# Performance work log

Hardware: AMD Instinct MI355X
Metric: run time of the kernel (lower is better)

## Reference

```python
import jax, jax.numpy as jnp
import numpy as np

TROPICAL_ZERO = jnp.float32(-1e38)  # tropical additive identity (acts as -inf)


def setup_inputs() -> dict:
    key = jax.random.key(0)
    k_x, k_w = jax.random.split(key)
    B, IN, OUT = 4096, 256, 256
    x = jax.random.normal(k_x, (B, IN), dtype=jnp.float32)
    # weight = log(rand + 1e-6), matching nn.Parameter init in the torch module
    weight = jnp.log(jax.random.uniform(k_w, (OUT, IN), dtype=jnp.float32) + 1e-6)
    bias = jnp.zeros((OUT,), dtype=jnp.float32)
    return {"x": x, "weight": weight, "bias": bias}


def reference(x, weight, bias):
    # Tropical (max-plus) matmul: out[b, j] = max_k (x[b, k] + w[j, k]) + bias[j]
    # restricted to 'non-tropical-zero' products; if all products are tropical
    # zero, the output stays TROPICAL_ZERO (no bias added), as in the torch loop.
    products = x[:, None, :] + weight[None, :, :]          # [B, out, in]
    mask = products > TROPICAL_ZERO                        # [B, out, in]
    masked = jnp.where(mask, products, -jnp.inf)
    max_val = jnp.max(masked, axis=-1)                     # [B, out]
    any_valid = jnp.any(mask, axis=-1)                     # [B, out]
    out = jnp.where(any_valid, max_val + bias[None, :], TROPICAL_ZERO)
    return out
```

## Files before the change

kernel.cpp:

```cpp
#include <hip/hip_runtime.h>


#define TZERO -1e38f

constexpr int K    = 256;
constexpr int N    = 256;
constexpr int Bdim = 4096;
constexpr int BN   = 32;
constexpr int SKW  = 8;
constexpr int KQ   = K / SKW;
constexpr int NT   = 64 * SKW;
constexpr int RPB  = 64;

__global__ __launch_bounds__(NT, 4)
void tropical_kernel(const float* __restrict__ x, const float* __restrict__ w,
                     const float* __restrict__ bias, float* __restrict__ out)
{
    __shared__ float red[SKW][BN][65];

    const int t    = threadIdx.x;
    const int lane = t & 63;
    const int wave = __builtin_amdgcn_readfirstlane(t >> 6);
    const int row0 = blockIdx.x * RPB;
    const int col0 = blockIdx.y * BN;

    float xr[KQ];
    {
        const float* xp = x + (size_t)(row0 + lane) * K + wave * KQ;
#pragma unroll
        for (int i4 = 0; i4 < KQ / 4; ++i4) {
            const float4 v = *reinterpret_cast<const float4*>(xp + i4 * 4);
            xr[i4 * 4 + 0] = v.x;
            xr[i4 * 4 + 1] = v.y;
            xr[i4 * 4 + 2] = v.z;
            xr[i4 * 4 + 3] = v.w;
        }
    }

    const float* wp0 = w + (size_t)col0 * K + wave * KQ;

#pragma unroll 2
    for (int j = 0; j < BN; ++j) {
        const float* wp = wp0 + (size_t)j * K;
        float m = -__builtin_inff();
#pragma unroll
        for (int i4 = 0; i4 < KQ / 4; ++i4) {
            const float4 wv = *reinterpret_cast<const float4*>(wp + i4 * 4);
            const float t0 = xr[i4 * 4 + 0] + wv.x;
            const float t1 = xr[i4 * 4 + 1] + wv.y;
            const float t2 = xr[i4 * 4 + 2] + wv.z;
            const float t3 = xr[i4 * 4 + 3] + wv.w;
            m = fmaxf(fmaxf(m, t0), t1);
            m = fmaxf(fmaxf(m, t2), t3);
        }
        red[wave][j][lane] = m;
    }
    __syncthreads();

    const int jj = t & 31;
    const int r0 = t >> 5;
    const float bj = bias[col0 + jj];
#pragma unroll
    for (int i = 0; i < 4; ++i) {
        const int r = r0 + 16 * i;
        float m = red[0][jj][r];
#pragma unroll
        for (int q = 1; q < SKW; ++q) m = fmaxf(m, red[q][jj][r]);
        out[(size_t)(row0 + r) * N + col0 + jj] = (m > TZERO) ? m + bj : TZERO;
    }
}

extern "C" void kernel_launch(void* const* d_in, const int* in_sizes, int n_in,
                              void* d_out, int out_size, void* d_ws, size_t ws_size,
                              hipStream_t stream) {
    const float* x  = (const float*)d_in[0];
    const float* w  = (const float*)d_in[1];
    const float* b  = (const float*)d_in[2];
    float* out      = (float*)d_out;

    dim3 grid(Bdim / RPB, N / BN);
    tropical_kernel<<<grid, NT, 0, stream>>>(x, w, b, out);
}
```

Baseline: 74.67 us.

## Shrink column tile to eight and fully unroll per-block column loop

```diff
diff --git a/kernel.cpp b/kernel.cpp
--- a/kernel.cpp
+++ b/kernel.cpp
@@ -6,68 +6,73 @@
 constexpr int K    = 256;
 constexpr int N    = 256;
 constexpr int Bdim = 4096;
-constexpr int BN   = 32;
-constexpr int SKW  = 8;
-constexpr int KQ   = K / SKW;
-constexpr int NT   = 64 * SKW;
-constexpr int RPB  = 64;
+constexpr int ROWS = 64;
+constexpr int J    = 8;
+constexpr int SK   = 8;
+constexpr int KC   = K / SK;
+constexpr int NT   = 64 * SK;
 
-__global__ __launch_bounds__(NT, 4)
+__global__ __launch_bounds__(NT, 8)
 void tropical_kernel(const float* __restrict__ x, const float* __restrict__ w,
                      const float* __restrict__ bias, float* __restrict__ out)
 {
-    __shared__ float red[SKW][BN][65];
+    __shared__ float red[SK][ROWS][J + 1];
 
     const int t    = threadIdx.x;
     const int lane = t & 63;
-    const int wave = __builtin_amdgcn_readfirstlane(t >> 6);
-    const int row0 = blockIdx.x * RPB;
-    const int col0 = blockIdx.y * BN;
+    const int kc   = __builtin_amdgcn_readfirstlane(t >> 6);
+    const int row0 = blockIdx.x * ROWS;
+    const int col0 = blockIdx.y * J;
 
-    float xr[KQ];
+    float xv[KC];
     {
-        const float* xp = x + (size_t)(row0 + lane) * K + wave * KQ;
+        const float* xp = x + (size_t)(row0 + lane) * K + kc * KC;
 #pragma unroll
-        for (int i4 = 0; i4 < KQ / 4; ++i4) {
+        for (int i4 = 0; i4 < KC / 4; ++i4) {
             const float4 v = *reinterpret_cast<const float4*>(xp + i4 * 4);
-            xr[i4 * 4 + 0] = v.x;
-            xr[i4 * 4 + 1] = v.y;
-            xr[i4 * 4 + 2] = v.z;
-            xr[i4 * 4 + 3] = v.w;
+            xv[i4 * 4 + 0] = v.x;
+            xv[i4 * 4 + 1] = v.y;
+            xv[i4 * 4 + 2] = v.z;
+            xv[i4 * 4 + 3] = v.w;
         }
     }
 
-    const float* wp0 = w + (size_t)col0 * K + wave * KQ;
+    float acc[J];
+#pragma unroll
+    for (int j = 0; j < J; ++j) acc[j] = -__builtin_inff();
 
-#pragma unroll 2
-    for (int j = 0; j < BN; ++j) {
-        const float* wp = wp0 + (size_t)j * K;
-        float m = -__builtin_inff();
+    const float* wbase = w + (size_t)col0 * K + kc * KC;
 #pragma unroll
-        for (int i4 = 0; i4 < KQ / 4; ++i4) {
-            const float4 wv = *reinterpret_cast<const float4*>(wp + i4 * 4);
-            const float t0 = xr[i4 * 4 + 0] + wv.x;
-            const float t1 = xr[i4 * 4 + 1] + wv.y;
-            const float t2 = xr[i4 * 4 + 2] + wv.z;
-            const float t3 = xr[i4 * 4 + 3] + wv.w;
+    for (int j = 0; j < J; ++j) {
+        const float* wp = wbase + (size_t)j * K;
+        float m = acc[j];
+#pragma unroll
+        for (int i4 = 0; i4 < KC / 4; ++i4) {
+            const float w0 = wp[i4 * 4 + 0];
+            const float w1 = wp[i4 * 4 + 1];
+            const float w2 = wp[i4 * 4 + 2];
+            const float w3 = wp[i4 * 4 + 3];
+            const float t0 = xv[i4 * 4 + 0] + w0;
+            const float t1 = xv[i4 * 4 + 1] + w1;
+            const float t2 = xv[i4 * 4 + 2] + w2;
+            const float t3 = xv[i4 * 4 + 3] + w3;
             m = fmaxf(fmaxf(m, t0), t1);
             m = fmaxf(fmaxf(m, t2), t3);
         }
-        red[wave][j][lane] = m;
+        acc[j] = m;
     }
+
+#pragma unroll
+    for (int j = 0; j < J; ++j) red[kc][lane][j] = acc[j];
     __syncthreads();
 
-    const int jj = t & 31;
-    const int r0 = t >> 5;
+    const int jj = t & (J - 1);
+    const int r  = t >> 3;
+    float m = red[0][r][jj];
+#pragma unroll
+    for (int q = 1; q < SK; ++q) m = fmaxf(m, red[q][r][jj]);
     const float bj = bias[col0 + jj];
-#pragma unroll
-    for (int i = 0; i < 4; ++i) {
-        const int r = r0 + 16 * i;
-        float m = red[0][jj][r];
-#pragma unroll
-        for (int q = 1; q < SKW; ++q) m = fmaxf(m, red[q][jj][r]);
-        out[(size_t)(row0 + r) * N + col0 + jj] = (m > TZERO) ? m + bj : TZERO;
-    }
+    out[(size_t)(row0 + r) * N + col0 + jj] = (m > TZERO) ? m + bj : TZERO;
 }
 
 extern "C" void kernel_launch(void* const* d_in, const int* in_sizes, int n_in,
@@ -78,6 +83,6 @@
     const float* b  = (const float*)d_in[2];
     float* out      = (float*)d_out;
 
-    dim3 grid(Bdim / RPB, N / BN);
+    dim3 grid(Bdim / ROWS, N / J);
     tropical_kernel<<<grid, NT, 0, stream>>>(x, w, b, out);
 }
```

New measurement: 76.61 us. +2.6%, slower.
